# Kernel tuning notes

Hardware: AMD Instinct MI355X
Metric: run time of the kernel (lower is better)

## Reference

```python
import jax, jax.numpy as jnp
import numpy as np

VOCAB, EMBED, FILT, LABELS = 30522, 256, 256, 50
B, S = 32, 4096

def setup_inputs() -> dict:
    key = jax.random.key(0)
    k0, k1, k2, k3, k4 = jax.random.split(key, 5)
    return {
        "input_ids": jax.random.randint(k0, (B, S), 0, VOCAB),
        "emb_table": jax.random.normal(k1, (VOCAB, EMBED), dtype=jnp.float32) * 0.02,
        "conv_w": jax.random.normal(k2, (FILT, EMBED, 4), dtype=jnp.float32) * 0.05,  # (out_ch, in_ch, k)
        "conv_b": jnp.zeros((FILT,), dtype=jnp.float32),
        "U_w": jax.random.normal(k3, (LABELS, FILT), dtype=jnp.float32) * 0.05,  # torch Linear weight layout
        "final_w": jax.random.normal(k4, (LABELS, FILT), dtype=jnp.float32) * 0.05,
        "final_b": jnp.zeros((LABELS,), dtype=jnp.float32),
    }

def reference(input_ids, emb_table, conv_w, conv_b, U_w, final_w, final_b):
    # Embedding lookup: (B, S, E) -> NCH layout (B, E, S)
    x = jnp.take(emb_table, input_ids, axis=0).transpose(0, 2, 1)
    # Conv1d(kernel=4, padding=2): output length S+1
    h = jax.lax.conv_general_dilated(
        x, conv_w, window_strides=(1,), padding=[(2, 2)],
        dimension_numbers=("NCH", "OIH", "NCH"))
    H = jnp.tanh(h + conv_b[None, :, None]).transpose(0, 2, 1)  # (B, S+1, F)
    # Per-label attention: softmax over the sequence dimension
    scores = jnp.einsum("bsf,lf->bsl", H, U_w)          # (B, S+1, L)
    alpha = jax.nn.softmax(scores, axis=1)
    m = jnp.einsum("bsl,bsf->blf", alpha, H)             # (B, L, F)
    logits = jnp.sum(m * final_w[None], axis=2) + final_b  # (B, L)
    return logits
```

## Files before the change

### kernel.cpp

```cpp
#include <hip/hip_runtime.h>
#include <hip/hip_bf16.h>
#include <stdint.h>

#define BDIM 32
#define SDIM 4096
#define SP1  4097
#define EDIM 256
#define FDIM 256
#define LDIM 50
#define TTILE 128
#define NT    32

typedef __attribute__((ext_vector_type(8))) short bf16x8v;
typedef __attribute__((ext_vector_type(4))) float f32x4;

__device__ __forceinline__ unsigned short f2bf(float f) {
    union { float f; uint32_t u; } v; v.f = f;
    uint32_t u = v.u;
    uint32_t r = (u + 0x7fffu + ((u >> 16) & 1u)) >> 16;
    return (unsigned short)r;
}

__device__ __forceinline__ float tanh_fast(float x) {
    float e = __expf(2.0f * x);
    float r = __builtin_amdgcn_rcpf(e + 1.0f);
    return fmaf(-2.0f, r, 1.0f);
}

__device__ __forceinline__ uint32_t pack_bf2(float lo, float hi) {
    union { __hip_bfloat162 v; uint32_t u; } cv;
    cv.v = __halves2bfloat162(__float2bfloat16(lo), __float2bfloat16(hi));
    return cv.u;
}

__device__ __forceinline__ void load_lds16(const void* g, uint32_t* l) {
    __builtin_amdgcn_global_load_lds(
        (const __attribute__((address_space(1))) uint32_t*)g,
        (__attribute__((address_space(3))) uint32_t*)l, 16, 0, 0);
}

__global__ void prep_all(const float* __restrict__ emb, const float* __restrict__ conv_w,
                         const float* __restrict__ U_w, const float* __restrict__ final_w,
                         unsigned short* __restrict__ embb, unsigned short* __restrict__ Wb2,
                         unsigned short* __restrict__ W2k, float* __restrict__ Wt01,
                         uint32_t* __restrict__ zp)
{
    int o = blockIdx.x * 256 + threadIdx.x;
    size_t eo = (size_t)o * 8;
    if (eo < (size_t)30522 * 256) {
        float4 v0 = *(const float4*)(emb + eo);
        float4 v1 = *(const float4*)(emb + eo + 4);
        union { unsigned short u[8]; uint4 q; } pk;
        pk.u[0] = f2bf(v0.x); pk.u[1] = f2bf(v0.y); pk.u[2] = f2bf(v0.z); pk.u[3] = f2bf(v0.w);
        pk.u[4] = f2bf(v1.x); pk.u[5] = f2bf(v1.y); pk.u[6] = f2bf(v1.z); pk.u[7] = f2bf(v1.w);
        *(uint4*)(embb + eo) = pk.q;
    }
    if (o < 262144) {
        int kk = o & 1023, f = o >> 10;
        int e = kk & 255, k = kk >> 8;
        int g = kk >> 5, h4 = (kk >> 3) & 3, j = kk & 7;
        Wb2[((size_t)(g * 4 + h4) * 256 + f) * 8 + j] = f2bf(conv_w[f * 1024 + e * 4 + k]);
    }
    if (o < 32768) {
        int j = o & 7, c = (o >> 3) & 127, g = o >> 10;
        int k = g * 8 + j, l = c & 63;
        float v = 0.f;
        if (l < LDIM) v = (c < 64) ? U_w[l * FDIM + k] : final_w[l * FDIM + k];
        W2k[o] = f2bf(v);
    }
    if (o < 65536) {
        int f = o & 255, e = o >> 8;
        Wt01[(size_t)o * 2]     = conv_w[f * 1024 + e * 4];
        Wt01[(size_t)o * 2 + 1] = conv_w[f * 1024 + e * 4 + 1];
    }
    if (o < 128) zp[o] = 0;
}

__global__ __launch_bounds__(256, 2) void fused_kernel(
    const int* __restrict__ ids, const unsigned short* __restrict__ embb,
    const unsigned short* __restrict__ Wb2, const float* __restrict__ conv_b,
    const unsigned short* __restrict__ W2k, const uint32_t* __restrict__ zp,
    float* __restrict__ part)
{
    __shared__ uint32_t xs[132 * 128];

    const int tid  = threadIdx.x;
    const int lane = tid & 63;
    const int wid  = tid >> 6;
    const int b    = blockIdx.y;
    const int tile = blockIdx.x;
    const int t0   = tile * TTILE;
    const int l15  = lane & 15;
    const int hi4  = lane >> 4;
    const int q    = lane & 31;
    const int half = lane >> 5;
    const int wm   = wid & 1;
    const int wn   = wid >> 1;

    {
        int nid[17];
        #pragma unroll
        for (int j = 0; j < 17; ++j) {
            int r0 = wid * 2 + j * 8;
            int r  = r0 + half;
            int p  = t0 - 2 + r;
            nid[j] = -1;
            if (r0 < 131 && r < 131 && (unsigned)p < SDIM)
                nid[j] = ids[b * SDIM + p];
        }
        const unsigned short* zs = (const unsigned short*)zp + q * 8;
        #pragma unroll
        for (int j = 0; j < 17; ++j) {
            int r0 = wid * 2 + j * 8;
            if (r0 >= 131) continue;
            int r = r0 + half;
            const unsigned short* s = (nid[j] >= 0)
                ? embb + (size_t)nid[j] * EDIM + (((uint32_t)(q * 16) ^ ((uint32_t)(r & 7) << 4)) >> 1)
                : zs;
            load_lds16(s, &xs[r0 * 128]);
        }
    }
    __syncthreads();

    const int fbase = wm * 128;
    const int tnb   = wn * 64;
    const unsigned short* afbase = Wb2 + (size_t)(hi4 * 256 + fbase + l15) * 8;

    f32x4 acc[8][4];
    #pragma unroll
    for (int a = 0; a < 8; ++a)
        #pragma unroll
        for (int n = 0; n < 4; ++n) acc[a][n] = (f32x4){0.f, 0.f, 0.f, 0.f};

    bf16x8v afc[8];
    #pragma unroll
    for (int a = 0; a < 8; ++a) afc[a] = *(const bf16x8v*)(afbase + a * 128);

    #pragma unroll 1
    for (int k = 0; k < 4; ++k) {
        uint32_t bb[4];
        #pragma unroll
        for (int n = 0; n < 4; ++n) {
            int r = tnb + n * 16 + l15 + k;
            bb[n] = (uint32_t)(r * 512) ^ (uint32_t)(hi4 * 16) ^ (uint32_t)((r & 7) << 4);
        }
        const unsigned short* afg = afbase + (size_t)k * 65536;
        #pragma unroll
        for (int es = 0; es < 8; ++es) {
            const unsigned short* nxt = (es < 7)
                ? (afg + (size_t)(es + 1) * 8192)
                : (afbase + (size_t)((k + 1) & 3) * 65536);
            bf16x8v afn[8];
            #pragma unroll
            for (int a = 0; a < 8; ++a) afn[a] = *(const bf16x8v*)(nxt + a * 128);

            bf16x8v bfr[4];
            #pragma unroll
            for (int n = 0; n < 4; ++n)
                bfr[n] = *(const bf16x8v*)((const char*)xs + (bb[n] ^ (uint32_t)(es * 64)));

            __builtin_amdgcn_s_setprio(1);
            #pragma unroll
            for (int a = 0; a < 8; ++a)
                #pragma unroll
                for (int n = 0; n < 4; ++n)
                    acc[a][n] = __builtin_amdgcn_mfma_f32_16x16x32_bf16(afc[a], bfr[n], acc[a][n], 0, 0, 0);
            __builtin_amdgcn_s_setprio(0);

            #pragma unroll
            for (int a = 0; a < 8; ++a) afc[a] = afn[a];
        }
    }
    __syncthreads();

    #pragma unroll
    for (int n = 0; n < 4; ++n) {
        int tl = tnb + n * 16 + l15;
        uint32_t hb = (uint32_t)(tl * 512) ^ (uint32_t)(hi4 * 8)
                    ^ (uint32_t)(fbase * 2) ^ (uint32_t)((tl & 7) << 4);
        #pragma unroll
        for (int a = 0; a < 8; ++a) {
            float4 cb = *(const float4*)(conv_b + fbase + a * 16 + hi4 * 4);
            f32x4 d = acc[a][n];
            uint2 pk;
            pk.x = pack_bf2(tanh_fast(d[0] + cb.x), tanh_fast(d[1] + cb.y));
            pk.y = pack_bf2(tanh_fast(d[2] + cb.z), tanh_fast(d[3] + cb.w));
            *(uint2*)((char*)xs + (hb ^ (uint32_t)(a * 32))) = pk;
        }
    }
    __syncthreads();

    const int cbase = wid * 16;
    f32x4 p2[8][2];
    #pragma unroll
    for (int m = 0; m < 8; ++m) { p2[m][0] = (f32x4){0,0,0,0}; p2[m][1] = (f32x4){0,0,0,0}; }

    uint32_t pb[8];
    #pragma unroll
    for (int m = 0; m < 8; ++m) {
        int sl = m * 16 + l15;
        pb[m] = (uint32_t)(sl * 512) ^ (uint32_t)(hi4 * 16) ^ (uint32_t)((sl & 7) << 4);
    }
    const unsigned short* wp0 = W2k + (size_t)(hi4 * 128 + cbase + l15) * 8;

    #pragma unroll
    for (int step = 0; step < 8; ++step) {
        bf16x8v ha[8], w2[2];
        #pragma unroll
        for (int m = 0; m < 8; ++m)
            ha[m] = *(const bf16x8v*)((const char*)xs + (pb[m] ^ (uint32_t)(step * 64)));
        w2[0] = *(const bf16x8v*)(wp0 + step * 4096);
        w2[1] = *(const bf16x8v*)(wp0 + 512 + step * 4096);
        __builtin_amdgcn_s_setprio(1);
        #pragma unroll
        for (int m = 0; m < 8; ++m) {
            p2[m][0] = __builtin_amdgcn_mfma_f32_16x16x32_bf16(ha[m], w2[0], p2[m][0], 0, 0, 0);
            p2[m][1] = __builtin_amdgcn_mfma_f32_16x16x32_bf16(ha[m], w2[1], p2[m][1], 0, 0, 0);
        }
        __builtin_amdgcn_s_setprio(0);
    }

    float mx = -1e30f;
    #pragma unroll
    for (int m = 0; m < 8; ++m)
        #pragma unroll
        for (int i = 0; i < 4; ++i)
            mx = fmaxf(mx, p2[m][0][i]);
    float se = 0.f, st = 0.f;
    #pragma unroll
    for (int m = 0; m < 8; ++m)
        #pragma unroll
        for (int i = 0; i < 4; ++i) {
            float e = __expf(p2[m][0][i] - mx);
            se += e;
            st += e * p2[m][1][i];
        }
    #pragma unroll
    for (int d = 16; d <= 32; d <<= 1) {
        float mo  = __shfl_xor(mx, d);
        float seo = __shfl_xor(se, d);
        float sto = __shfl_xor(st, d);
        float M  = fmaxf(mx, mo);
        float w0 = __expf(mx - M), w1 = __expf(mo - M);
        se = se * w0 + seo * w1;
        st = st * w0 + sto * w1;
        mx = M;
    }
    if (lane < 16) {
        int l = cbase + l15;
        if (l < LDIM) {
            size_t o = (((size_t)b * NT + tile) * LDIM + l) * 3;
            part[o] = mx; part[o + 1] = se; part[o + 2] = st;
        }
    }
}

__global__ __launch_bounds__(256) void final_kernel(
    const int* __restrict__ ids, const float* __restrict__ emb,
    const float* __restrict__ Wt01, const float* __restrict__ conv_b,
    const float* __restrict__ U_w, const float* __restrict__ final_w,
    const float* __restrict__ part, const float* __restrict__ final_b,
    float* __restrict__ out)
{
    __shared__ float x0[EDIM], x1[EDIM], hsh[FDIM], rsc[256], rtv[256];
    const int b = blockIdx.x, t = threadIdx.x;

    {
        int id0 = ids[b * SDIM + 4094];
        int id1 = ids[b * SDIM + 4095];
        x0[t] = emb[(size_t)id0 * EDIM + t];
        x1[t] = emb[(size_t)id1 * EDIM + t];
    }
    __syncthreads();

    {
        const float2* wt = (const float2*)Wt01;
        float a0 = 0.f, a1 = 0.f, a2 = 0.f, a3 = 0.f;
        #pragma unroll 4
        for (int e = 0; e < 256; e += 4) {
            float2 w0 = wt[(e + 0) * 256 + t];
            float2 w1 = wt[(e + 1) * 256 + t];
            float2 w2 = wt[(e + 2) * 256 + t];
            float2 w3 = wt[(e + 3) * 256 + t];
            a0 = fmaf(w0.x, x0[e + 0], fmaf(w0.y, x1[e + 0], a0));
            a1 = fmaf(w1.x, x0[e + 1], fmaf(w1.y, x1[e + 1], a1));
            a2 = fmaf(w2.x, x0[e + 2], fmaf(w2.y, x1[e + 2], a2));
            a3 = fmaf(w3.x, x0[e + 3], fmaf(w3.y, x1[e + 3], a3));
        }
        hsh[t] = tanhf(conv_b[t] + ((a0 + a1) + (a2 + a3)));
    }
    __syncthreads();

    {
        const int l = t & 63, c = t >> 6;
        float sc = 0.f, tv = 0.f;
        if (l < LDIM) {
            const float4* uw = (const float4*)(U_w + (size_t)l * FDIM + c * 64);
            const float4* fw = (const float4*)(final_w + (size_t)l * FDIM + c * 64);
            const float4* hh = (const float4*)(hsh + c * 64);
            #pragma unroll
            for (int i = 0; i < 16; ++i) {
                float4 h = hh[i], u = uw[i], w = fw[i];
                sc = fmaf(h.x, u.x, fmaf(h.y, u.y, fmaf(h.z, u.z, fmaf(h.w, u.w, sc))));
                tv = fmaf(h.x, w.x, fmaf(h.y, w.y, fmaf(h.z, w.z, fmaf(h.w, w.w, tv))));
            }
        }
        rsc[t] = sc; rtv[t] = tv;
    }
    __syncthreads();

    if (t < LDIM) {
        float sc = rsc[t] + rsc[t + 64] + rsc[t + 128] + rsc[t + 192];
        float tv = rtv[t] + rtv[t + 64] + rtv[t + 128] + rtv[t + 192];
        float mx = sc, se = 1.0f, st = tv;
        for (int c = 0; c < NT; ++c) {
            size_t o = (((size_t)b * NT + c) * LDIM + t) * 3;
            float mo = part[o], seo = part[o + 1], sto = part[o + 2];
            float M  = fmaxf(mx, mo);
            float w0 = __expf(mx - M), w1 = __expf(mo - M);
            se = se * w0 + seo * w1;
            st = st * w0 + sto * w1;
            mx = M;
        }
        out[b * LDIM + t] = st / se + final_b[t];
    }
}

extern "C" void kernel_launch(void* const* d_in, const int* in_sizes, int n_in,
                              void* d_out, int out_size, void* d_ws, size_t ws_size,
                              hipStream_t stream)
{
    const int*   ids     = (const int*)d_in[0];
    const float* emb     = (const float*)d_in[1];
    const float* conv_w  = (const float*)d_in[2];
    const float* conv_b  = (const float*)d_in[3];
    const float* U_w     = (const float*)d_in[4];
    const float* final_w = (const float*)d_in[5];
    const float* final_b = (const float*)d_in[6];

    char* ws = (char*)d_ws;
    size_t offE  = 0;
    size_t szE   = (size_t)30522 * 256 * 2;
    size_t offWb = offE + szE;
    size_t szWb  = 256 * 1024 * 2;
    size_t offW2 = offWb + szWb;
    size_t szW2  = 32768 * 2;
    size_t offWt = offW2 + szW2;
    size_t szWt  = 65536 * 2 * 4;
    size_t offZ  = offWt + szWt;
    size_t szZ   = 512;
    size_t offP  = offZ + szZ;

    unsigned short* embb = (unsigned short*)(ws + offE);
    unsigned short* Wb2  = (unsigned short*)(ws + offWb);
    unsigned short* W2k  = (unsigned short*)(ws + offW2);
    float*          Wt01 = (float*)(ws + offWt);
    uint32_t*       zp   = (uint32_t*)(ws + offZ);
    float*          prt  = (float*)(ws + offP);

    prep_all<<<3816, 256, 0, stream>>>(emb, conv_w, U_w, final_w, embb, Wb2, W2k, Wt01, zp);
    fused_kernel<<<dim3(NT, BDIM), 256, 0, stream>>>(ids, embb, Wb2, conv_b, W2k, zp, prt);
    final_kernel<<<BDIM, 256, 0, stream>>>(ids, emb, Wt01, conv_b, U_w, final_w,
                                           prt, final_b, (float*)d_out);
}
```

Baseline: 101.3 us.

## Switch conv and attention GEMMs to 32x32x16 MFMA with new weight layouts

Replaces the 16x16x32 bf16 MFMA tiles with 32x32x16 tiles in both the convolution GEMM and the score/value GEMM. Each wave now owns 64 filters across all 128 timesteps, and the second stage splits the sequence rows into two halves, so twice as many softmax partials are written. The weight prep layouts are rearranged to match, and the final kernel merges 64 partials per batch row instead of 32. The aim is fewer MFMA issues per unit of work and fewer A-fragment loads per block. The cost is larger accumulator register tiles and more partial-merge work at the end.

```diff
diff --git a/kernel.cpp b/kernel.cpp
--- a/kernel.cpp
+++ b/kernel.cpp
@@ -11,8 +11,8 @@
 #define TTILE 128
 #define NT    32
 
-typedef __attribute__((ext_vector_type(8))) short bf16x8v;
-typedef __attribute__((ext_vector_type(4))) float f32x4;
+typedef __attribute__((ext_vector_type(8)))  short bf16x8v;
+typedef __attribute__((ext_vector_type(16))) float f32x16;
 
 __device__ __forceinline__ unsigned short f2bf(float f) {
     union { float f; uint32_t u; } v; v.f = f;
@@ -41,8 +41,8 @@
 
 __global__ void prep_all(const float* __restrict__ emb, const float* __restrict__ conv_w,
                          const float* __restrict__ U_w, const float* __restrict__ final_w,
-                         unsigned short* __restrict__ embb, unsigned short* __restrict__ Wb2,
-                         unsigned short* __restrict__ W2k, float* __restrict__ Wt01,
+                         unsigned short* __restrict__ embb, unsigned short* __restrict__ Wb3,
+                         unsigned short* __restrict__ W2k3, float* __restrict__ Wt01,
                          uint32_t* __restrict__ zp)
 {
     int o = blockIdx.x * 256 + threadIdx.x;
@@ -56,17 +56,18 @@
         *(uint4*)(embb + eo) = pk.q;
     }
     if (o < 262144) {
-        int kk = o & 1023, f = o >> 10;
-        int e = kk & 255, k = kk >> 8;
-        int g = kk >> 5, h4 = (kk >> 3) & 3, j = kk & 7;
-        Wb2[((size_t)(g * 4 + h4) * 256 + f) * 8 + j] = f2bf(conv_w[f * 1024 + e * 4 + k]);
+        int j = o & 7, f = (o >> 3) & 255, half = (o >> 11) & 1, g16 = o >> 12;
+        int kg = g16 * 16 + half * 8 + j;
+        int e = kg & 255, tap = kg >> 8;
+        Wb3[o] = f2bf(conv_w[f * 1024 + e * 4 + tap]);
     }
     if (o < 32768) {
-        int j = o & 7, c = (o >> 3) & 127, g = o >> 10;
-        int k = g * 8 + j, l = c & 63;
+        int j = o & 7, cg = (o >> 3) & 127, half = (o >> 10) & 1, kc = o >> 11;
+        int k = kc * 16 + half * 8 + j;
         float v = 0.f;
-        if (l < LDIM) v = (c < 64) ? U_w[l * FDIM + k] : final_w[l * FDIM + k];
-        W2k[o] = f2bf(v);
+        if (cg < 64) { if (cg < LDIM) v = U_w[cg * FDIM + k]; }
+        else         { int cl = cg - 64; if (cl < LDIM) v = final_w[cl * FDIM + k]; }
+        W2k3[o] = f2bf(v);
     }
     if (o < 65536) {
         int f = o & 255, e = o >> 8;
@@ -78,8 +79,8 @@
 
 __global__ __launch_bounds__(256, 2) void fused_kernel(
     const int* __restrict__ ids, const unsigned short* __restrict__ embb,
-    const unsigned short* __restrict__ Wb2, const float* __restrict__ conv_b,
-    const unsigned short* __restrict__ W2k, const uint32_t* __restrict__ zp,
+    const unsigned short* __restrict__ Wb3, const float* __restrict__ conv_b,
+    const unsigned short* __restrict__ W2k3, const uint32_t* __restrict__ zp,
     float* __restrict__ part)
 {
     __shared__ uint32_t xs[132 * 128];
@@ -90,12 +91,10 @@
     const int b    = blockIdx.y;
     const int tile = blockIdx.x;
     const int t0   = tile * TTILE;
-    const int l15  = lane & 15;
-    const int hi4  = lane >> 4;
+    const int l31  = lane & 31;
+    const int hi5  = lane >> 5;
     const int q    = lane & 31;
     const int half = lane >> 5;
-    const int wm   = wid & 1;
-    const int wn   = wid >> 1;
 
     {
         int nid[17];
@@ -122,134 +121,143 @@
     }
     __syncthreads();
 
-    const int fbase = wm * 128;
-    const int tnb   = wn * 64;
-    const unsigned short* afbase = Wb2 + (size_t)(hi4 * 256 + fbase + l15) * 8;
-
-    f32x4 acc[8][4];
-    #pragma unroll
-    for (int a = 0; a < 8; ++a)
-        #pragma unroll
-        for (int n = 0; n < 4; ++n) acc[a][n] = (f32x4){0.f, 0.f, 0.f, 0.f};
-
-    bf16x8v afc[8];
-    #pragma unroll
-    for (int a = 0; a < 8; ++a) afc[a] = *(const bf16x8v*)(afbase + a * 128);
+    const int fbase = wid * 64;
+    const unsigned short* afbase = Wb3 + ((size_t)hi5 * 256 + fbase + l31) * 8;
+
+    f32x16 acc[2][4];
+    #pragma unroll
+    for (int a = 0; a < 2; ++a)
+        #pragma unroll
+        for (int n = 0; n < 4; ++n)
+            acc[a][n] = (f32x16){0,0,0,0,0,0,0,0,0,0,0,0,0,0,0,0};
+
+    bf16x8v afc[2];
+    afc[0] = *(const bf16x8v*)(afbase);
+    afc[1] = *(const bf16x8v*)(afbase + 256);
 
     #pragma unroll 1
-    for (int k = 0; k < 4; ++k) {
+    for (int tap = 0; tap < 4; ++tap) {
         uint32_t bb[4];
         #pragma unroll
         for (int n = 0; n < 4; ++n) {
-            int r = tnb + n * 16 + l15 + k;
-            bb[n] = (uint32_t)(r * 512) ^ (uint32_t)(hi4 * 16) ^ (uint32_t)((r & 7) << 4);
-        }
-        const unsigned short* afg = afbase + (size_t)k * 65536;
-        #pragma unroll
-        for (int es = 0; es < 8; ++es) {
-            const unsigned short* nxt = (es < 7)
-                ? (afg + (size_t)(es + 1) * 8192)
-                : (afbase + (size_t)((k + 1) & 3) * 65536);
-            bf16x8v afn[8];
-            #pragma unroll
-            for (int a = 0; a < 8; ++a) afn[a] = *(const bf16x8v*)(nxt + a * 128);
+            int r = n * 32 + l31 + tap;
+            bb[n] = (uint32_t)(r * 512) ^ (uint32_t)(hi5 * 16) ^ (uint32_t)((r & 7) << 4);
+        }
+        const unsigned short* afg = afbase + (size_t)tap * 65536;
+        #pragma unroll
+        for (int ke = 0; ke < 16; ++ke) {
+            const unsigned short* nxt = (ke < 15)
+                ? (afg + (size_t)(ke + 1) * 4096)
+                : (afbase + (size_t)((tap + 1) & 3) * 65536);
+            bf16x8v afn0 = *(const bf16x8v*)(nxt);
+            bf16x8v afn1 = *(const bf16x8v*)(nxt + 256);
 
             bf16x8v bfr[4];
             #pragma unroll
             for (int n = 0; n < 4; ++n)
-                bfr[n] = *(const bf16x8v*)((const char*)xs + (bb[n] ^ (uint32_t)(es * 64)));
+                bfr[n] = *(const bf16x8v*)((const char*)xs + (bb[n] ^ (uint32_t)(ke * 32)));
 
             __builtin_amdgcn_s_setprio(1);
             #pragma unroll
-            for (int a = 0; a < 8; ++a)
-                #pragma unroll
-                for (int n = 0; n < 4; ++n)
-                    acc[a][n] = __builtin_amdgcn_mfma_f32_16x16x32_bf16(afc[a], bfr[n], acc[a][n], 0, 0, 0);
+            for (int n = 0; n < 4; ++n) {
+                acc[0][n] = __builtin_amdgcn_mfma_f32_32x32x16_bf16(afc[0], bfr[n], acc[0][n], 0, 0, 0);
+                acc[1][n] = __builtin_amdgcn_mfma_f32_32x32x16_bf16(afc[1], bfr[n], acc[1][n], 0, 0, 0);
+            }
             __builtin_amdgcn_s_setprio(0);
 
+            afc[0] = afn0; afc[1] = afn1;
+        }
+    }
+    __syncthreads();
+
+    float4 cbv[2][4];
+    #pragma unroll
+    for (int a = 0; a < 2; ++a)
+        #pragma unroll
+        for (int g = 0; g < 4; ++g)
+            cbv[a][g] = *(const float4*)(conv_b + fbase + a * 32 + g * 8 + hi5 * 4);
+    #pragma unroll
+    for (int n = 0; n < 4; ++n) {
+        int tl = n * 32 + l31;
+        uint32_t hb = (uint32_t)(tl * 512) ^ (uint32_t)(fbase * 2)
+                    ^ (uint32_t)(hi5 * 8) ^ (uint32_t)((tl & 7) << 4);
+        #pragma unroll
+        for (int a = 0; a < 2; ++a) {
+            f32x16 d = acc[a][n];
             #pragma unroll
-            for (int a = 0; a < 8; ++a) afc[a] = afn[a];
-        }
-    }
-    __syncthreads();
-
-    #pragma unroll
-    for (int n = 0; n < 4; ++n) {
-        int tl = tnb + n * 16 + l15;
-        uint32_t hb = (uint32_t)(tl * 512) ^ (uint32_t)(hi4 * 8)
-                    ^ (uint32_t)(fbase * 2) ^ (uint32_t)((tl & 7) << 4);
-        #pragma unroll
-        for (int a = 0; a < 8; ++a) {
-            float4 cb = *(const float4*)(conv_b + fbase + a * 16 + hi4 * 4);
-            f32x4 d = acc[a][n];
-            uint2 pk;
-            pk.x = pack_bf2(tanh_fast(d[0] + cb.x), tanh_fast(d[1] + cb.y));
-            pk.y = pack_bf2(tanh_fast(d[2] + cb.z), tanh_fast(d[3] + cb.w));
-            *(uint2*)((char*)xs + (hb ^ (uint32_t)(a * 32))) = pk;
-        }
-    }
-    __syncthreads();
-
-    const int cbase = wid * 16;
-    f32x4 p2[8][2];
-    #pragma unroll
-    for (int m = 0; m < 8; ++m) { p2[m][0] = (f32x4){0,0,0,0}; p2[m][1] = (f32x4){0,0,0,0}; }
-
-    uint32_t pb[8];
-    #pragma unroll
-    for (int m = 0; m < 8; ++m) {
-        int sl = m * 16 + l15;
-        pb[m] = (uint32_t)(sl * 512) ^ (uint32_t)(hi4 * 16) ^ (uint32_t)((sl & 7) << 4);
-    }
-    const unsigned short* wp0 = W2k + (size_t)(hi4 * 128 + cbase + l15) * 8;
-
-    #pragma unroll
-    for (int step = 0; step < 8; ++step) {
-        bf16x8v ha[8], w2[2];
-        #pragma unroll
-        for (int m = 0; m < 8; ++m)
-            ha[m] = *(const bf16x8v*)((const char*)xs + (pb[m] ^ (uint32_t)(step * 64)));
-        w2[0] = *(const bf16x8v*)(wp0 + step * 4096);
-        w2[1] = *(const bf16x8v*)(wp0 + 512 + step * 4096);
+            for (int g = 0; g < 4; ++g) {
+                float4 cb = cbv[a][g];
+                uint2 pk;
+                pk.x = pack_bf2(tanh_fast(d[4*g+0] + cb.x), tanh_fast(d[4*g+1] + cb.y));
+                pk.y = pack_bf2(tanh_fast(d[4*g+2] + cb.z), tanh_fast(d[4*g+3] + cb.w));
+                *(uint2*)((char*)xs + (hb ^ (uint32_t)(a * 64) ^ (uint32_t)(g * 16))) = pk;
+            }
+        }
+    }
+    __syncthreads();
+
+    const int lb = wid & 1;
+    const int rh = wid >> 1;
+    f32x16 ps[2], pt[2];
+    #pragma unroll
+    for (int m = 0; m < 2; ++m) {
+        ps[m] = (f32x16){0,0,0,0,0,0,0,0,0,0,0,0,0,0,0,0};
+        pt[m] = (f32x16){0,0,0,0,0,0,0,0,0,0,0,0,0,0,0,0};
+    }
+    uint32_t pb[2];
+    #pragma unroll
+    for (int m = 0; m < 2; ++m) {
+        int sl = rh * 64 + m * 32 + l31;
+        pb[m] = (uint32_t)(sl * 512) ^ (uint32_t)(hi5 * 16) ^ (uint32_t)((sl & 7) << 4);
+    }
+    const unsigned short* wpb = W2k3 + ((size_t)hi5 * 128 + lb * 32 + l31) * 8;
+
+    #pragma unroll
+    for (int kc = 0; kc < 16; ++kc) {
+        bf16x8v ha[2], w2s, w2t;
+        #pragma unroll
+        for (int m = 0; m < 2; ++m)
+            ha[m] = *(const bf16x8v*)((const char*)xs + (pb[m] ^ (uint32_t)(kc * 32)));
+        w2s = *(const bf16x8v*)(wpb + kc * 2048);
+        w2t = *(const bf16x8v*)(wpb + kc * 2048 + 512);
         __builtin_amdgcn_s_setprio(1);
         #pragma unroll
-        for (int m = 0; m < 8; ++m) {
-            p2[m][0] = __builtin_amdgcn_mfma_f32_16x16x32_bf16(ha[m], w2[0], p2[m][0], 0, 0, 0);
-            p2[m][1] = __builtin_amdgcn_mfma_f32_16x16x32_bf16(ha[m], w2[1], p2[m][1], 0, 0, 0);
+        for (int m = 0; m < 2; ++m) {
+            ps[m] = __builtin_amdgcn_mfma_f32_32x32x16_bf16(ha[m], w2s, ps[m], 0, 0, 0);
+            pt[m] = __builtin_amdgcn_mfma_f32_32x32x16_bf16(ha[m], w2t, pt[m], 0, 0, 0);
         }
         __builtin_amdgcn_s_setprio(0);
     }
 
     float mx = -1e30f;
     #pragma unroll
-    for (int m = 0; m < 8; ++m)
-        #pragma unroll
-        for (int i = 0; i < 4; ++i)
-            mx = fmaxf(mx, p2[m][0][i]);
+    for (int m = 0; m < 2; ++m)
+        #pragma unroll
+        for (int i = 0; i < 16; ++i)
+            mx = fmaxf(mx, ps[m][i]);
     float se = 0.f, st = 0.f;
     #pragma unroll
-    for (int m = 0; m < 8; ++m)
-        #pragma unroll
-        for (int i = 0; i < 4; ++i) {
-            float e = __expf(p2[m][0][i] - mx);
+    for (int m = 0; m < 2; ++m)
+        #pragma unroll
+        for (int i = 0; i < 16; ++i) {
+            float e = __expf(ps[m][i] - mx);
             se += e;
-            st += e * p2[m][1][i];
-        }
-    #pragma unroll
-    for (int d = 16; d <= 32; d <<= 1) {
-        float mo  = __shfl_xor(mx, d);
-        float seo = __shfl_xor(se, d);
-        float sto = __shfl_xor(st, d);
+            st += e * pt[m][i];
+        }
+    {
+        float mo  = __shfl_xor(mx, 32);
+        float seo = __shfl_xor(se, 32);
+        float sto = __shfl_xor(st, 32);
         float M  = fmaxf(mx, mo);
         float w0 = __expf(mx - M), w1 = __expf(mo - M);
         se = se * w0 + seo * w1;
         st = st * w0 + sto * w1;
         mx = M;
     }
-    if (lane < 16) {
-        int l = cbase + l15;
+    if (lane < 32) {
+        int l = lb * 32 + lane;
         if (l < LDIM) {
-            size_t o = (((size_t)b * NT + tile) * LDIM + l) * 3;
+            size_t o = ((((size_t)b * NT + tile) * 2 + rh) * LDIM + l) * 3;
             part[o] = mx; part[o + 1] = se; part[o + 2] = st;
         }
     }
@@ -313,8 +321,8 @@
         float sc = rsc[t] + rsc[t + 64] + rsc[t + 128] + rsc[t + 192];
         float tv = rtv[t] + rtv[t + 64] + rtv[t + 128] + rtv[t + 192];
         float mx = sc, se = 1.0f, st = tv;
-        for (int c = 0; c < NT; ++c) {
-            size_t o = (((size_t)b * NT + c) * LDIM + t) * 3;
+        for (int c = 0; c < 2 * NT; ++c) {
+            size_t o = (((size_t)b * 2 * NT + c) * LDIM + t) * 3;
             float mo = part[o], seo = part[o + 1], sto = part[o + 2];
             float M  = fmaxf(mx, mo);
             float w0 = __expf(mx - M), w1 = __expf(mo - M);
@@ -342,7 +350,7 @@
     size_t offE  = 0;
     size_t szE   = (size_t)30522 * 256 * 2;
     size_t offWb = offE + szE;
-    size_t szWb  = 256 * 1024 * 2;
+    size_t szWb  = 262144 * 2;
     size_t offW2 = offWb + szWb;
     size_t szW2  = 32768 * 2;
     size_t offWt = offW2 + szW2;
@@ -352,14 +360,14 @@
     size_t offP  = offZ + szZ;
 
     unsigned short* embb = (unsigned short*)(ws + offE);
-    unsigned short* Wb2  = (unsigned short*)(ws + offWb);
-    unsigned short* W2k  = (unsigned short*)(ws + offW2);
+    unsigned short* Wb3  = (unsigned short*)(ws + offWb);
+    unsigned short* W2k3 = (unsigned short*)(ws + offW2);
     float*          Wt01 = (float*)(ws + offWt);
     uint32_t*       zp   = (uint32_t*)(ws + offZ);
     float*          prt  = (float*)(ws + offP);
 
-    prep_all<<<3816, 256, 0, stream>>>(emb, conv_w, U_w, final_w, embb, Wb2, W2k, Wt01, zp);
-    fused_kernel<<<dim3(NT, BDIM), 256, 0, stream>>>(ids, embb, Wb2, conv_b, W2k, zp, prt);
+    prep_all<<<3816, 256, 0, stream>>>(emb, conv_w, U_w, final_w, embb, Wb3, W2k3, Wt01, zp);
+    fused_kernel<<<dim3(NT, BDIM), 256, 0, stream>>>(ids, embb, Wb3, conv_b, W2k3, zp, prt);
     final_kernel<<<BDIM, 256, 0, stream>>>(ids, emb, Wt01, conv_b, U_w, final_w,
                                            prt, final_b, (float*)d_out);
 }
```

Measured after the change: 114.9 us. +13.3%, slower.
